# Kernel tuning notes

Measured on AMD Instinct MI355X. Metric: run time of the kernel, lower is better.

Reference implementation:

```python
import jax, jax.numpy as jnp
import numpy as np

B, T, S = 32, 200, 256          # batch, decoder steps, encoder (memory) length
L = 512                          # latent_dims
U = 2 * L                        # LSTM units / attention units / attention_layer_size
E = 512                          # encoder memory feature dim
M = 80                           # mel_bins


def setup_inputs() -> dict:
    key = jax.random.key(0)
    ks = jax.random.split(key, 16)
    s = 0.05
    inputs = jax.random.normal(ks[0], (B, T, M), jnp.float32)
    memory = jax.random.normal(ks[1], (B, S, E), jnp.float32)
    # pre-net: Dense(2L, relu) -> Dropout -> Dense(L, relu) -> Dropout
    W1 = jax.random.normal(ks[2], (M, 2 * L), jnp.float32) * s
    b1 = jnp.zeros((2 * L,), jnp.float32)
    W2 = jax.random.normal(ks[3], (2 * L, L), jnp.float32) * s
    b2 = jnp.zeros((L,), jnp.float32)
    # LSTMCell(2L): input = concat(prenet_out [L], attention [U=2L]) -> 3L
    Wx = jax.random.normal(ks[4], (3 * L, 4 * U), jnp.float32) * s
    Wh = jax.random.normal(ks[5], (U, 4 * U), jnp.float32) * s
    b_lstm = jnp.zeros((4 * U,), jnp.float32)
    # Bahdanau attention (units=U): memory_layer, query_layer (no bias), score vector v
    Wm = jax.random.normal(ks[6], (E, U), jnp.float32) * s
    Wq = jax.random.normal(ks[7], (U, U), jnp.float32) * s
    v_att = jax.random.normal(ks[8], (U,), jnp.float32) * s
    # attention_layer (Dense, no bias): concat(cell_output [U], context [E]) -> U
    Wa = jax.random.normal(ks[9], (U + E, U), jnp.float32) * s
    # output projection to mel bins
    Wp = jax.random.normal(ks[10], (U, M), jnp.float32) * s
    bp = jnp.zeros((M,), jnp.float32)
    return dict(inputs=inputs, memory=memory, W1=W1, b1=b1, W2=W2, b2=b2,
                Wx=Wx, Wh=Wh, b_lstm=b_lstm, Wm=Wm, Wq=Wq, v_att=v_att,
                Wa=Wa, Wp=Wp, bp=bp)


def reference(inputs, memory, W1, b1, W2, b2, Wx, Wh, b_lstm, Wm, Wq, v_att, Wa, Wp, bp):
    # pre-net (inference: dropout is identity)
    x = jax.nn.relu(inputs @ W1 + b1)
    x = jax.nn.relu(x @ W2 + b2)                       # [B,T,L]
    keys = memory @ Wm                                 # precomputed attention keys [B,S,U]

    def step(carry, xt):
        h, c, attn = carry
        cell_in = jnp.concatenate([xt, attn], axis=-1)  # [B, 3L]
        z = cell_in @ Wx + h @ Wh + b_lstm              # [B, 4U]
        i, f, g, o = jnp.split(z, 4, axis=-1)
        c_new = jax.nn.sigmoid(f) * c + jax.nn.sigmoid(i) * jnp.tanh(g)
        h_new = jax.nn.sigmoid(o) * jnp.tanh(c_new)
        # Bahdanau additive attention
        q = h_new @ Wq                                  # [B,U]
        score = jnp.einsum('u,bsu->bs', v_att, jnp.tanh(keys + q[:, None, :]))
        align = jax.nn.softmax(score, axis=-1)          # [B,S]
        ctx = jnp.einsum('bs,bse->be', align, memory)   # [B,E]
        attn_new = jnp.concatenate([h_new, ctx], axis=-1) @ Wa  # [B,U]
        return (h_new, c_new, attn_new), attn_new

    init = (jnp.zeros((B, U), x.dtype), jnp.zeros((B, U), x.dtype), jnp.zeros((B, U), x.dtype))
    xs = jnp.swapaxes(x, 0, 1)                          # [T,B,L]
    (h, c, attn), ys = jax.lax.scan(step, init, xs)
    outs = jnp.swapaxes(ys, 0, 1)                       # [B,T,U]
    mel = outs @ Wp + bp                                # [B,T,M]
    return (mel, h, c, attn)
```

## Files before the change

kernel.cpp:

```cpp
#include <hip/hip_runtime.h>


typedef unsigned short us16;
typedef unsigned int u32;
typedef unsigned long long u64;
typedef __attribute__((ext_vector_type(8))) short bf16x8;
typedef __attribute__((ext_vector_type(4))) float f32x4;

#define MFMA16 __builtin_amdgcn_mfma_f32_16x16x32_bf16
#define AGT __HIP_MEMORY_SCOPE_AGENT

__device__ __forceinline__ us16 f2bf(float f){
  u32 u = __builtin_bit_cast(u32, f);
  u += 0x7fffu + ((u >> 16) & 1u);
  return (us16)(u >> 16);
}
__device__ __forceinline__ float bf2f(us16 h){
  return __builtin_bit_cast(float, ((u32)h) << 16);
}
__device__ __forceinline__ float h2f(us16 u){
  _Float16 h = __builtin_bit_cast(_Float16, u); return (float)h;
}
__device__ __forceinline__ us16 f2h(float f){
  _Float16 h = (_Float16)f; return __builtin_bit_cast(us16, h);
}
__device__ __forceinline__ void split3(float v, us16& s0, us16& s1, us16& s2){
  s0 = f2bf(v); float r = v - bf2f(s0);
  s1 = f2bf(r); r -= bf2f(s1);
  s2 = f2bf(r);
}
__device__ __forceinline__ float tanh_fast(float x){
  float e = __expf(-2.f * fmaxf(x, -40.f));
  return (1.f - e) / (1.f + e);
}
__device__ __forceinline__ float sigf(float x){
  return 1.f / (1.f + __expf(-x));
}

__device__ __forceinline__ u32 aload32(const u32* p){
  return __hip_atomic_load(p, __ATOMIC_RELAXED, AGT);
}
__device__ __forceinline__ void astore16(us16* p, us16 v){
  __hip_atomic_store(p, v, __ATOMIC_RELAXED, AGT);
}
__device__ __forceinline__ void astoref(float* p, float v){
  __hip_atomic_store(p, v, __ATOMIC_RELAXED, AGT);
}
__device__ __forceinline__ void sigflag(u32* p, u32 v){
  __hip_atomic_store(p, v, __ATOMIC_RELAXED, AGT);
}
__device__ __forceinline__ void aaddf(float* p, float v){
  __hip_atomic_fetch_add(p, v, __ATOMIC_RELAXED, AGT);
}
__device__ __forceinline__ bf16x8 ld16(const us16* p){
  return *(const bf16x8*)p;
}
__device__ __forceinline__ bf16x8 pin_reg(bf16x8 v){
  f32x4 t = __builtin_bit_cast(f32x4, v);
  asm volatile("" : "+v"(t));
  return __builtin_bit_cast(bf16x8, t);
}
__device__ __forceinline__ void f32_frag3(const float* p, float rs,
                                          bf16x8& f0, bf16x8& f1, bf16x8& f2){
  float4 t0 = *(const float4*)p;
  float4 t1 = *(const float4*)(p + 4);
  float tf[8] = {t0.x, t0.y, t0.z, t0.w, t1.x, t1.y, t1.z, t1.w};
#pragma unroll
  for (int i = 0; i < 8; ++i){
    float v = tf[i] * rs;
    us16 s0, s1, s2; split3(v, s0, s1, s2);
    f0[i] = (short)s0; f1[i] = (short)s1; f2[i] = (short)s2;
  }
}

#define OFF_WTA    0ull
#define OFF_WQT    50331648ull
#define OFF_X2P    56623104ull
#define OFF_KEYH   76283904ull
#define OFF_KEYL   93061120ull
#define OFF_X1     76283904ull
#define OFF_HIST   109838336ull
#define OFF_HPR    129597440ull
#define OFF_UCR    169115648ull
#define OFF_SR     182288384ull
#define OFF_CB     182314112ull
#define OFF_HF     182445184ull
#define OFF_WAPN   182576256ull
#define OFF_BPERM  182822016ull
#define OFF_ARR    182838400ull
#define OFF_QR     182859776ull
#define TOTAL_WS   209084416ull

#define WTPL 8388608ull
#define WQPL 1048576ull
#define X2PL 3276800ull

__global__ void k_zero_init(u32* hpr0, float* ucr, float* sr, float* cbuf, u32* arr){
  u32 id = blockIdx.x * 256u + threadIdx.x;
  const u32 gs = 65536u;
  for (u32 i = id; i < 49152u;   i += gs) hpr0[i] = 0u;
  for (u32 i = id; i < 3293184u; i += gs) ucr[i]  = 0.f;
  for (u32 i = id; i < 6432u;    i += gs) sr[i]   = (i < 32u) ? 1.f : 0.f;
  for (u32 i = id; i < 32768u;   i += gs) cbuf[i] = 0.f;
  for (u32 i = id; i < 5120u;    i += gs) arr[i]  = 0u;
}

__global__ void k_bperm(const float* __restrict__ bl, float* __restrict__ bpm){
  int c = blockIdx.x * 256 + threadIdx.x;
  if (c < 4096) bpm[((c & 1023) << 2) | (c >> 10)] = bl[c];
}

__global__ void k_transp3(const float* __restrict__ src, us16* __restrict__ dst,
                          int srows, int scols, int ldd, long long pstride, int perm){
  __shared__ float tile[32][33];
  int bx = blockIdx.x * 32, by = blockIdx.y * 32;
  int tx = threadIdx.x & 31, ty = threadIdx.x >> 5;
#pragma unroll
  for (int i = 0; i < 4; ++i){
    int r = by + ty + i * 8, c = bx + tx;
    tile[ty + i * 8][tx] = (r < srows && c < scols) ? src[(size_t)r * scols + c] : 0.f;
  }
  __syncthreads();
#pragma unroll
  for (int i = 0; i < 4; ++i){
    int c = bx + ty + i * 8;
    int r = by + tx;
    if (c < scols && r < srows){
      int oc = perm ? (((c & 1023) << 2) | (c >> 10)) : c;
      float v = tile[tx][ty + i * 8];
      us16 s0, s1, s2; split3(v, s0, s1, s2);
      size_t base = (size_t)oc * ldd + r;
      dst[base] = s0; dst[(size_t)pstride + base] = s1; dst[2ull * pstride + base] = s2;
    }
  }
}

template<int NP, int AF, int BF>
__global__ void __launch_bounds__(256)
k_gemm3(const void* __restrict__ Ap, const void* __restrict__ Bp, void* __restrict__ outp,
        int M, int N, int K, int mode, const float* __restrict__ aux, int ldd){
  __shared__ us16 At[NP][128][72];
  __shared__ us16 Bt[NP][64][72];
  const int tid = threadIdx.x, wv = tid >> 6, lane = tid & 63;
  const int r0 = lane & 15, kg = lane >> 4;
  const int rb = blockIdx.x * 128, cb = blockIdx.y * 64;
  f32x4 acc[2][4];
#pragma unroll
  for (int a = 0; a < 2; ++a)
#pragma unroll
    for (int b = 0; b < 4; ++b) acc[a][b] = (f32x4){0.f, 0.f, 0.f, 0.f};

  const int nkt = (K + 63) >> 6;
  for (int kt = 0; kt < nkt; ++kt){
    const int kb = kt * 64;
    for (int e = tid; e < 8192; e += 256){
      int r = e >> 6, k = e & 63, ga = rb + r, gk = kb + k;
      bool ok = (ga < M) && (gk < K);
      if constexpr (AF){
        float v = ok ? ((const float*)Ap)[(size_t)ga * K + gk] : 0.f;
        us16 s0, s1, s2; split3(v, s0, s1, s2);
        At[0][r][k] = s0;
        if constexpr (NP == 3){ At[1][r][k] = s1; At[2][r][k] = s2; }
      } else {
        At[0][r][k] = ok ? ((const us16*)Ap)[(size_t)ga * K + gk] : (us16)0;
      }
    }
    for (int e = tid; e < 4096; e += 256){
      int kr = e >> 6, c = e & 63, gk = kb + kr, gc = cb + c;
      bool ok = (gk < K) && (gc < N);
      if constexpr (BF){
        float v = ok ? ((const float*)Bp)[(size_t)gk * N + gc] : 0.f;
        us16 s0, s1, s2; split3(v, s0, s1, s2);
        Bt[0][c][kr] = s0;
        if constexpr (NP == 3){ Bt[1][c][kr] = s1; Bt[2][c][kr] = s2; }
      } else {
        Bt[0][c][kr] = ok ? ((const us16*)Bp)[(size_t)gk * N + gc] : (us16)0;
      }
    }
    __syncthreads();
#pragma unroll
    for (int kk = 0; kk < 64; kk += 32){
      bf16x8 af[NP][2];
#pragma unroll
      for (int p = 0; p < NP; ++p){
        af[p][0] = *(const bf16x8*)&At[p][wv * 32 + r0][kk + kg * 8];
        af[p][1] = *(const bf16x8*)&At[p][wv * 32 + 16 + r0][kk + kg * 8];
      }
#pragma unroll
      for (int cf = 0; cf < 4; ++cf){
        bf16x8 bv[NP];
#pragma unroll
        for (int p = 0; p < NP; ++p) bv[p] = *(const bf16x8*)&Bt[p][cf * 16 + r0][kk + kg * 8];
#pragma unroll
        for (int rf = 0; rf < 2; ++rf){
          acc[rf][cf] = MFMA16(af[0][rf], bv[0], acc[rf][cf], 0, 0, 0);
          if constexpr (NP == 3){
            acc[rf][cf] = MFMA16(af[0][rf], bv[1], acc[rf][cf], 0, 0, 0);
            acc[rf][cf] = MFMA16(af[1][rf], bv[0], acc[rf][cf], 0, 0, 0);
            acc[rf][cf] = MFMA16(af[0][rf], bv[2], acc[rf][cf], 0, 0, 0);
            acc[rf][cf] = MFMA16(af[1][rf], bv[1], acc[rf][cf], 0, 0, 0);
            acc[rf][cf] = MFMA16(af[2][rf], bv[0], acc[rf][cf], 0, 0, 0);
          }
        }
      }
    }
    __syncthreads();
  }
  us16* o16 = (us16*)outp; float* of = (float*)outp;
#pragma unroll
  for (int rf = 0; rf < 2; ++rf)
#pragma unroll
    for (int cf = 0; cf < 4; ++cf)
#pragma unroll
      for (int i = 0; i < 4; ++i){
        int r = rb + wv * 32 + rf * 16 + kg * 4 + i;
        int c = cb + cf * 16 + r0;
        if (r >= M || c >= N) continue;
        float v = acc[rf][cf][i];
        if (mode == 0){
          of[(size_t)r * ldd + c] = fmaxf(v + aux[c], 0.f);
        } else if (mode == 1){
          v = fmaxf(v + aux[c], 0.f);
          us16 s0, s1, s2; split3(v, s0, s1, s2);
          size_t b2 = (size_t)r * ldd + c;
          o16[b2] = s0; o16[X2PL + b2] = s1; o16[2 * X2PL + b2] = s2;
        } else if (mode == 2){
          us16 hh = f2h(v); float rem = v - h2f(hh); us16 hl = f2h(rem);
          size_t b2 = (size_t)r * 1024 + c;
          o16[b2] = hh; o16[WTPL + b2] = hl;
        } else if (mode == 3){
          float w = v + (r < 1024 ? aux[(size_t)r * 4096 + c] : 0.f);
          int pc = (c & 1023) * 4 + (c >> 10);
          us16 s0, s1, s2; split3(w, s0, s1, s2);
          size_t b2 = (size_t)pc * 2048 + 512 + r;
          o16[b2] = s0; o16[WTPL + b2] = s1; o16[2 * WTPL + b2] = s2;
        } else if (mode == 4){
          o16[(size_t)r * ldd + c] = f2bf(v);
        } else if (mode == 5){
          of[((size_t)(r & 31) * 200 + (r >> 5)) * 80 + c] = v + aux[c];
        } else {
          of[(size_t)r * ldd + c] = v;
        }
      }
}

__device__ __forceinline__ void gbar3(u32* arr, u32 ep, int tid, int blk){
  asm volatile("s_waitcnt vmcnt(0)" ::: "memory");
  __syncthreads();
  if (blk == 0){
    if (tid > 0 && tid < 256)
      while (aload32(&arr[tid * 16]) < ep) __builtin_amdgcn_s_sleep(2);
    __syncthreads();
    if (tid < 8) sigflag(&arr[4096 + tid * 32], ep);
    __syncthreads();
  } else {
    if (tid == 0){
      sigflag(&arr[blk * 16], ep);
      const int g = blk >> 5;
      while (aload32(&arr[4096 + g * 32]) < ep) __builtin_amdgcn_s_sleep(2);
      __builtin_amdgcn_sched_barrier(0);
    }
    __syncthreads();
  }
}

struct CoopA {
  const us16 *wta, *wqt, *x2p, *kh, *kl;
  const float *mem, *vatt, *bperm;
  us16 *hpr;
  float *ucr, *sr, *qr, *cbuf, *hf32;
  u32 *arr;
};

__global__ void __launch_bounds__(512, 1) k_coop(CoopA a){
  __shared__ us16 khi[32][1024];
  __shared__ us16 klo[32][1024];
  __shared__ float zp[8][512];
  __shared__ float esc[32];
  __shared__ float rs_lds[32];

  __builtin_amdgcn_fence(__ATOMIC_ACQUIRE, "agent");

  const int tid = threadIdx.x, blk = blockIdx.x;
  const int wv = tid >> 6, lane = tid & 63;
  const int r0 = lane & 15, kg = lane >> 4;
  const int cb_b = blk >> 3, cb_s0 = (blk & 7) * 32;
  const int colbase = blk * 16;
  const int u0 = lane * 16;

  bf16x8 wr[8][3];
#pragma unroll
  for (int ks = 0; ks < 8; ++ks){
    const size_t wb = (size_t)(colbase + r0) * 2048 + (size_t)wv * 256 + ks * 32 + kg * 8;
#pragma unroll
    for (int p = 0; p < 3; ++p)
      wr[ks][p] = pin_reg(*(const bf16x8*)&a.wta[(size_t)p * WTPL + wb]);
  }

  {
    const size_t kbase = ((size_t)(cb_b * 256 + cb_s0)) * 1024;
    for (int i = tid; i < 4096; i += 512){
      int r = i >> 7, c8 = (i & 127) * 8;
      *(bf16x8*)&khi[r][c8] = *(const bf16x8*)&a.kh[kbase + (size_t)r * 1024 + c8];
      *(bf16x8*)&klo[r][c8] = *(const bf16x8*)&a.kl[kbase + (size_t)r * 1024 + c8];
    }
  }
  __syncthreads();

  u32 ep = 0;
  for (int t = 0; t < 200; ++t){
    {
      if (tid < 32) rs_lds[tid] = 1.f / a.sr[(size_t)t * 32 + tid];
      __syncthreads();
      f32x4 acc0 = (f32x4){0.f,0.f,0.f,0.f}, acc1 = acc0;
#pragma unroll
      for (int ks = 0; ks < 8; ++ks){
        const int kf = wv * 256 + ks * 32 + kg * 8;
        bf16x8 w0 = wr[ks][0], w1 = wr[ks][1], w2 = wr[ks][2];
        bf16x8 a00, a01, a02, a10, a11, a12;
        if (wv < 2){
          const size_t xb0 = ((size_t)r0 * 200 + t) * 512 + kf;
          const size_t xb1 = ((size_t)(r0 + 16) * 200 + t) * 512 + kf;
          a00 = *(const bf16x8*)&a.x2p[xb0];
          a01 = *(const bf16x8*)&a.x2p[X2PL + xb0];
          a02 = *(const bf16x8*)&a.x2p[2 * X2PL + xb0];
          a10 = *(const bf16x8*)&a.x2p[xb1];
          a11 = *(const bf16x8*)&a.x2p[X2PL + xb1];
          a12 = *(const bf16x8*)&a.x2p[2 * X2PL + xb1];
        } else if (wv < 6){
          const int hk = kf - 512;
          const us16* hb = a.hpr + (size_t)t * 98304;
          a00 = ld16(&hb[(size_t)r0 * 1024 + hk]);
          a01 = ld16(&hb[32768 + (size_t)r0 * 1024 + hk]);
          a02 = ld16(&hb[65536 + (size_t)r0 * 1024 + hk]);
          a10 = ld16(&hb[(size_t)(r0 + 16) * 1024 + hk]);
          a11 = ld16(&hb[32768 + (size_t)(r0 + 16) * 1024 + hk]);
          a12 = ld16(&hb[65536 + (size_t)(r0 + 16) * 1024 + hk]);
        } else {
          const int ek = kf - 1536;
          const float* up = a.ucr + (size_t)t * 16384 + (size_t)r0 * 512 + ek;
          f32_frag3(up,        rs_lds[r0],      a00, a01, a02);
          f32_frag3(up + 8192, rs_lds[r0 + 16], a10, a11, a12);
        }
        acc0 = MFMA16(a00, w0, acc0, 0,0,0); acc0 = MFMA16(a00, w1, acc0, 0,0,0);
        acc0 = MFMA16(a01, w0, acc0, 0,0,0); acc0 = MFMA16(a00, w2, acc0, 0,0,0);
        acc0 = MFMA16(a01, w1, acc0, 0,0,0); acc0 = MFMA16(a02, w0, acc0, 0,0,0);
        acc1 = MFMA16(a10, w0, acc1, 0,0,0); acc1 = MFMA16(a10, w1, acc1, 0,0,0);
        acc1 = MFMA16(a11, w0, acc1, 0,0,0); acc1 = MFMA16(a10, w2, acc1, 0,0,0);
        acc1 = MFMA16(a11, w1, acc1, 0,0,0); acc1 = MFMA16(a12, w0, acc1, 0,0,0);
      }
#pragma unroll
      for (int i = 0; i < 4; ++i){
        zp[wv][(kg * 4 + i) * 16 + r0]      = acc0[i];
        zp[wv][(16 + kg * 4 + i) * 16 + r0] = acc1[i];
      }
      __syncthreads();
      float z = 0.f;
#pragma unroll
      for (int w = 0; w < 8; ++w) z += zp[w][tid];
      z += a.bperm[colbase + (tid & 15)];
      __syncthreads();
      zp[0][tid] = z;
      __syncthreads();
      if (tid < 128){
        int b = tid >> 2, ul = tid & 3, u = blk * 4 + ul;
        float zi = zp[0][b * 16 + ul * 4 + 0];
        float zf = zp[0][b * 16 + ul * 4 + 1];
        float zg = zp[0][b * 16 + ul * 4 + 2];
        float zo = zp[0][b * 16 + ul * 4 + 3];
        float co = a.cbuf[b * 1024 + u];
        float cn = sigf(zf) * co + sigf(zi) * tanh_fast(zg);
        float hn = sigf(zo) * tanh_fast(cn);
        a.cbuf[b * 1024 + u] = cn;
        a.hf32[b * 1024 + u] = hn;
        us16 s0, s1, s2; split3(hn, s0, s1, s2);
        us16* hb = a.hpr + (size_t)(t + 1) * 98304;
        astore16(&hb[b * 1024 + u], s0);
        astore16(&hb[32768 + b * 1024 + u], s1);
        astore16(&hb[65536 + b * 1024 + u], s2);
      }
    }
    gbar3(a.arr, ++ep, tid, blk);

    if (blk < 64){
      f32x4 acc0 = (f32x4){0.f,0.f,0.f,0.f}, acc1 = acc0;
#pragma unroll
      for (int ks = 0; ks < 4; ++ks){
        const int kf = wv * 128 + ks * 32 + kg * 8;
        const size_t wb = (size_t)(colbase + r0) * 1024 + kf;
        bf16x8 w0 = *(const bf16x8*)&a.wqt[wb];
        bf16x8 w1 = *(const bf16x8*)&a.wqt[WQPL + wb];
        bf16x8 w2 = *(const bf16x8*)&a.wqt[2 * WQPL + wb];
        const us16* hb = a.hpr + (size_t)(t + 1) * 98304;
        bf16x8 a00 = ld16(&hb[(size_t)r0 * 1024 + kf]);
        bf16x8 a01 = ld16(&hb[32768 + (size_t)r0 * 1024 + kf]);
        bf16x8 a02 = ld16(&hb[65536 + (size_t)r0 * 1024 + kf]);
        bf16x8 a10 = ld16(&hb[(size_t)(r0 + 16) * 1024 + kf]);
        bf16x8 a11 = ld16(&hb[32768 + (size_t)(r0 + 16) * 1024 + kf]);
        bf16x8 a12 = ld16(&hb[65536 + (size_t)(r0 + 16) * 1024 + kf]);
        acc0 = MFMA16(a00, w0, acc0, 0,0,0); acc0 = MFMA16(a00, w1, acc0, 0,0,0);
        acc0 = MFMA16(a01, w0, acc0, 0,0,0); acc0 = MFMA16(a00, w2, acc0, 0,0,0);
        acc0 = MFMA16(a01, w1, acc0, 0,0,0); acc0 = MFMA16(a02, w0, acc0, 0,0,0);
        acc1 = MFMA16(a10, w0, acc1, 0,0,0); acc1 = MFMA16(a10, w1, acc1, 0,0,0);
        acc1 = MFMA16(a11, w0, acc1, 0,0,0); acc1 = MFMA16(a10, w2, acc1, 0,0,0);
        acc1 = MFMA16(a11, w1, acc1, 0,0,0); acc1 = MFMA16(a12, w0, acc1, 0,0,0);
      }
#pragma unroll
      for (int i = 0; i < 4; ++i){
        zp[wv][(kg * 4 + i) * 16 + r0]      = acc0[i];
        zp[wv][(16 + kg * 4 + i) * 16 + r0] = acc1[i];
      }
      __syncthreads();
      float q = 0.f;
#pragma unroll
      for (int w = 0; w < 8; ++w) q += zp[w][tid];
      astoref(&a.qr[(size_t)t * 32768 + (size_t)(tid >> 4) * 1024 + colbase + (tid & 15)], q);
    }
    gbar3(a.arr, ++ep, tid, blk);

    {
      float qv[16], vv[16];
      {
        const float* qp = a.qr + (size_t)t * 32768 + (size_t)cb_b * 1024 + u0;
        float4 q0 = *(const float4*)qp;
        float4 q1 = *(const float4*)(qp + 4);
        float4 q2 = *(const float4*)(qp + 8);
        float4 q3 = *(const float4*)(qp + 12);
        qv[0]=q0.x; qv[1]=q0.y; qv[2]=q0.z; qv[3]=q0.w;
        qv[4]=q1.x; qv[5]=q1.y; qv[6]=q1.z; qv[7]=q1.w;
        qv[8]=q2.x; qv[9]=q2.y; qv[10]=q2.z; qv[11]=q2.w;
        qv[12]=q3.x; qv[13]=q3.y; qv[14]=q3.z; qv[15]=q3.w;
        float4 v0 = *(const float4*)(a.vatt + u0);
        float4 v1 = *(const float4*)(a.vatt + u0 + 4);
        float4 v2 = *(const float4*)(a.vatt + u0 + 8);
        float4 v3 = *(const float4*)(a.vatt + u0 + 12);
        vv[0]=v0.x; vv[1]=v0.y; vv[2]=v0.z; vv[3]=v0.w;
        vv[4]=v1.x; vv[5]=v1.y; vv[6]=v1.z; vv[7]=v1.w;
        vv[8]=v2.x; vv[9]=v2.y; vv[10]=v2.z; vv[11]=v2.w;
        vv[12]=v3.x; vv[13]=v3.y; vv[14]=v3.z; vv[15]=v3.w;
      }
#pragma unroll
      for (int m = 0; m < 4; ++m){
        const int sl = wv * 4 + m;
        bf16x8 h0 = *(const bf16x8*)&khi[sl][u0];
        bf16x8 h1 = *(const bf16x8*)&khi[sl][u0 + 8];
        bf16x8 l0 = *(const bf16x8*)&klo[sl][u0];
        bf16x8 l1 = *(const bf16x8*)&klo[sl][u0 + 8];
        float part = 0.f;
#pragma unroll
        for (int j = 0; j < 8; ++j){
          float kva = h2f((us16)h0[j]) + h2f((us16)l0[j]);
          part += vv[j] * tanh_fast(kva + qv[j]);
          float kvb = h2f((us16)h1[j]) + h2f((us16)l1[j]);
          part += vv[8 + j] * tanh_fast(kvb + qv[8 + j]);
        }
#pragma unroll
        for (int off = 32; off; off >>= 1) part += __shfl_xor(part, off);
        if (lane == 0) esc[sl] = __expf(part);
      }
      __syncthreads();
      if (tid == 0){
        float bs = 0.f;
#pragma unroll
        for (int i = 0; i < 32; ++i) bs += esc[i];
        aaddf(&a.sr[(size_t)(t + 1) * 32 + cb_b], bs);
      }
      {
        float ac0 = 0.f, ac1 = 0.f, ac2 = 0.f, ac3 = 0.f;
        const float* mrow = a.mem + ((size_t)(cb_b * 256 + cb_s0)) * 512 + tid;
#pragma unroll
        for (int j = 0; j < 32; j += 4){
          ac0 += esc[j]     * mrow[(size_t)j * 512];
          ac1 += esc[j + 1] * mrow[(size_t)(j + 1) * 512];
          ac2 += esc[j + 2] * mrow[(size_t)(j + 2) * 512];
          ac3 += esc[j + 3] * mrow[(size_t)(j + 3) * 512];
        }
        aaddf(&a.ucr[(size_t)(t + 1) * 16384 + cb_b * 512 + tid], (ac0 + ac1) + (ac2 + ac3));
      }
    }
    gbar3(a.arr, ++ep, tid, blk);
  }
}

__global__ void k_hist(const us16* __restrict__ hpr, const float* __restrict__ ucr,
                       const float* __restrict__ sr, us16* __restrict__ hist){
  int row = blockIdx.x;
  int t = row >> 5, b = row & 31;
  float rs = 1.f / sr[(size_t)t * 32 + b];
  for (int c = threadIdx.x; c < 1536; c += 256){
    us16 v;
    if (c < 1024) v = hpr[(size_t)t * 98304 + b * 1024 + c];
    else          v = f2bf(ucr[(size_t)t * 16384 + b * 512 + (c - 1024)] * rs);
    hist[(size_t)row * 1536 + c] = v;
  }
}

__global__ void k_copy_hc(const float* __restrict__ h, const float* __restrict__ c,
                          float* __restrict__ out){
  int i = blockIdx.x * 256 + threadIdx.x;
  if (i < 32768){
    out[512000 + i] = h[i];
    out[544768 + i] = c[i];
  }
}

extern "C" void kernel_launch(void* const* d_in, const int* in_sizes, int n_in,
                              void* d_out, int out_size, void* d_ws, size_t ws_size,
                              hipStream_t stream){
  const float* inputs = (const float*)d_in[0];
  const float* memory = (const float*)d_in[1];
  const float* W1     = (const float*)d_in[2];
  const float* b1     = (const float*)d_in[3];
  const float* W2     = (const float*)d_in[4];
  const float* b2     = (const float*)d_in[5];
  const float* Wx     = (const float*)d_in[6];
  const float* Wh     = (const float*)d_in[7];
  const float* b_lstm = (const float*)d_in[8];
  const float* Wm     = (const float*)d_in[9];
  const float* Wq     = (const float*)d_in[10];
  const float* v_att  = (const float*)d_in[11];
  const float* Wa     = (const float*)d_in[12];
  const float* Wp     = (const float*)d_in[13];
  const float* bp     = (const float*)d_in[14];
  float* out = (float*)d_out;
  char* ws = (char*)d_ws;
  if (ws_size < TOTAL_WS) return;

  us16* WTA    = (us16*)(ws + OFF_WTA);
  us16* WQT    = (us16*)(ws + OFF_WQT);
  us16* X2P    = (us16*)(ws + OFF_X2P);
  us16* KEYH   = (us16*)(ws + OFF_KEYH);
  float* X1    = (float*)(ws + OFF_X1);
  us16* HIST   = (us16*)(ws + OFF_HIST);
  us16* HPR    = (us16*)(ws + OFF_HPR);
  float* UCR   = (float*)(ws + OFF_UCR);
  float* SR    = (float*)(ws + OFF_SR);
  float* QR    = (float*)(ws + OFF_QR);
  float* CB    = (float*)(ws + OFF_CB);
  float* HF    = (float*)(ws + OFF_HF);
  us16* WAPN   = (us16*)(ws + OFF_WAPN);
  float* BPM   = (float*)(ws + OFF_BPERM);
  u32*  ARR    = (u32*)(ws + OFF_ARR);

  k_zero_init<<<256, 256, 0, stream>>>((u32*)HPR, UCR, SR, CB, ARR);
  k_bperm<<<16, 256, 0, stream>>>(b_lstm, BPM);
  k_transp3<<<dim3(32, 32), 256, 0, stream>>>(Wq, WQT, 1024, 1024, 1024, (long long)WQPL, 0);
  k_transp3<<<dim3(128, 16), 256, 0, stream>>>(Wx, WTA, 512, 4096, 2048, (long long)WTPL, 1);

  k_gemm3<3,1,1><<<dim3(12, 64), 256, 0, stream>>>(Wa, Wx + (size_t)512 * 4096, WTA,
                                                   1536, 4096, 1024, 3, Wh, 0);
  k_gemm3<3,1,1><<<dim3(12, 2), 256, 0, stream>>>(Wa, Wp, WAPN, 1536, 80, 1024, 4, nullptr, 80);
  k_gemm3<3,1,1><<<dim3(50, 16), 256, 0, stream>>>(inputs, W1, X1, 6400, 1024, 80, 0, b1, 1024);
  k_gemm3<3,1,1><<<dim3(50, 8), 256, 0, stream>>>(X1, W2, X2P, 6400, 512, 1024, 1, b2, 512);
  k_gemm3<3,1,1><<<dim3(64, 16), 256, 0, stream>>>(memory, Wm, KEYH, 8192, 1024, 512, 2, nullptr, 1024);

  CoopA ca;
  ca.wta = WTA; ca.wqt = WQT; ca.x2p = X2P; ca.kh = KEYH; ca.kl = KEYH + WTPL;
  ca.mem = memory; ca.vatt = v_att; ca.bperm = BPM;
  ca.hpr = HPR; ca.ucr = UCR; ca.sr = SR;
  ca.qr = QR; ca.cbuf = CB; ca.hf32 = HF; ca.arr = ARR;
  void* args[] = {(void*)&ca};
  hipLaunchCooperativeKernel((const void*)k_coop, dim3(256), dim3(512), args, 0, stream);

  k_hist<<<6432, 256, 0, stream>>>(HPR, UCR, SR, HIST);
  k_gemm3<1,0,0><<<dim3(50, 2), 256, 0, stream>>>(HIST + (size_t)32 * 1536, WAPN, out,
                                                  6400, 80, 1536, 5, bp, 0);
  k_gemm3<1,0,1><<<dim3(1, 16), 256, 0, stream>>>(HIST + (size_t)200 * 32 * 1536, Wa,
                                                  out + 577536, 32, 1024, 1536, 6, nullptr, 1024);
  k_copy_hc<<<128, 256, 0, stream>>>(HF, CB, out);
}
```

Measured before the change: 12.58 ms.

## Split batch into two halves and pipeline phases with per-phase split barriers

Replaces the global three-phase barrier per timestep with arrive/wait counters per phase and per batch half. Each phase (LSTM gates, query projection, attention) runs on two 16-row halves, so one half's work can overlap with the other half's barrier latency. The Wq projection is now spread over 128 blocks instead of 64, and the attention block mapping is re-tiled to 16 positions by 2 batch groups. The cost is more barriers, MFMA tiles half as tall, which may underuse the matrix units, and extra LDS syncs.

```diff
diff --git a/kernel.cpp b/kernel.cpp
--- a/kernel.cpp
+++ b/kernel.cpp
@@ -88,12 +88,19 @@
 #define OFF_WAPN   182576256ull
 #define OFF_BPERM  182822016ull
 #define OFF_ARR    182838400ull
-#define OFF_QR     182859776ull
-#define TOTAL_WS   209084416ull
+#define OFF_QR     182870016ull
+#define TOTAL_WS   209094656ull
 
 #define WTPL 8388608ull
 #define WQPL 1048576ull
 #define X2PL 3276800ull
+
+#define SA0 0
+#define SA1 1
+#define SB0 2
+#define SB1 3
+#define SC0 4
+#define SC1 5
 
 __global__ void k_zero_init(u32* hpr0, float* ucr, float* sr, float* cbuf, u32* arr){
   u32 id = blockIdx.x * 256u + threadIdx.x;
@@ -102,7 +109,7 @@
   for (u32 i = id; i < 3293184u; i += gs) ucr[i]  = 0.f;
   for (u32 i = id; i < 6432u;    i += gs) sr[i]   = (i < 32u) ? 1.f : 0.f;
   for (u32 i = id; i < 32768u;   i += gs) cbuf[i] = 0.f;
-  for (u32 i = id; i < 5120u;    i += gs) arr[i]  = 0u;
+  for (u32 i = id; i < 2048u;    i += gs) arr[i]  = 0u;
 }
 
 __global__ void k_bperm(const float* __restrict__ bl, float* __restrict__ bpm){
@@ -244,24 +251,24 @@
       }
 }
 
-__device__ __forceinline__ void gbar3(u32* arr, u32 ep, int tid, int blk){
-  asm volatile("s_waitcnt vmcnt(0)" ::: "memory");
+__device__ __forceinline__ void arrv(u32* arr, int set, u32 ng, u32 ep, int tid, int blk){
   __syncthreads();
-  if (blk == 0){
-    if (tid > 0 && tid < 256)
-      while (aload32(&arr[tid * 16]) < ep) __builtin_amdgcn_s_sleep(2);
-    __syncthreads();
-    if (tid < 8) sigflag(&arr[4096 + tid * 32], ep);
-    __syncthreads();
-  } else {
-    if (tid == 0){
-      sigflag(&arr[blk * 16], ep);
-      const int g = blk >> 5;
-      while (aload32(&arr[4096 + g * 32]) < ep) __builtin_amdgcn_s_sleep(2);
-      __builtin_amdgcn_sched_barrier(0);
-    }
-    __syncthreads();
-  }
+  if (tid == 0){
+    int g = (blk >> 5) & 7;
+    u32 old = __hip_atomic_fetch_add(&arr[(set * 8 + g) * 32], 1u, __ATOMIC_RELAXED, AGT);
+    if (old == 32u * ep - 1u){
+      u32 r = __hip_atomic_fetch_add(&arr[(48 + set) * 32], 1u, __ATOMIC_RELAXED, AGT);
+      if (r == ng * ep - 1u)
+        sigflag(&arr[(56 + set) * 32], ep);
+    }
+  }
+}
+__device__ __forceinline__ void waitrel(u32* arr, int set, u32 ep, int tid){
+  if (tid == 0){
+    while (aload32(&arr[(56 + set) * 32]) < ep) __builtin_amdgcn_s_sleep(2);
+    __builtin_amdgcn_sched_barrier(0);
+  }
+  __syncthreads();
 }
 
 struct CoopA {
@@ -276,7 +283,7 @@
   __shared__ us16 khi[32][1024];
   __shared__ us16 klo[32][1024];
   __shared__ float zp[8][512];
-  __shared__ float esc[32];
+  __shared__ float esc[16];
   __shared__ float rs_lds[32];
 
   __builtin_amdgcn_fence(__ATOMIC_ACQUIRE, "agent");
@@ -284,7 +291,7 @@
   const int tid = threadIdx.x, blk = blockIdx.x;
   const int wv = tid >> 6, lane = tid & 63;
   const int r0 = lane & 15, kg = lane >> 4;
-  const int cb_b = blk >> 3, cb_s0 = (blk & 7) * 32;
+  const int b16 = blk >> 4, s0c = (blk & 15) * 16;
   const int colbase = blk * 16;
   const int u0 = lane * 16;
 
@@ -298,187 +305,191 @@
   }
 
   {
-    const size_t kbase = ((size_t)(cb_b * 256 + cb_s0)) * 1024;
     for (int i = tid; i < 4096; i += 512){
       int r = i >> 7, c8 = (i & 127) * 8;
-      *(bf16x8*)&khi[r][c8] = *(const bf16x8*)&a.kh[kbase + (size_t)r * 1024 + c8];
-      *(bf16x8*)&klo[r][c8] = *(const bf16x8*)&a.kl[kbase + (size_t)r * 1024 + c8];
+      int gb = (r < 16) ? b16 : (16 + b16);
+      int s  = s0c + (r & 15);
+      const size_t kb = ((size_t)(gb * 256 + s)) * 1024 + c8;
+      *(bf16x8*)&khi[r][c8] = *(const bf16x8*)&a.kh[kb];
+      *(bf16x8*)&klo[r][c8] = *(const bf16x8*)&a.kl[kb];
     }
   }
   __syncthreads();
 
-  u32 ep = 0;
-  for (int t = 0; t < 200; ++t){
-    {
-      if (tid < 32) rs_lds[tid] = 1.f / a.sr[(size_t)t * 32 + tid];
-      __syncthreads();
-      f32x4 acc0 = (f32x4){0.f,0.f,0.f,0.f}, acc1 = acc0;
-#pragma unroll
-      for (int ks = 0; ks < 8; ++ks){
-        const int kf = wv * 256 + ks * 32 + kg * 8;
-        bf16x8 w0 = wr[ks][0], w1 = wr[ks][1], w2 = wr[ks][2];
-        bf16x8 a00, a01, a02, a10, a11, a12;
-        if (wv < 2){
-          const size_t xb0 = ((size_t)r0 * 200 + t) * 512 + kf;
-          const size_t xb1 = ((size_t)(r0 + 16) * 200 + t) * 512 + kf;
-          a00 = *(const bf16x8*)&a.x2p[xb0];
-          a01 = *(const bf16x8*)&a.x2p[X2PL + xb0];
-          a02 = *(const bf16x8*)&a.x2p[2 * X2PL + xb0];
-          a10 = *(const bf16x8*)&a.x2p[xb1];
-          a11 = *(const bf16x8*)&a.x2p[X2PL + xb1];
-          a12 = *(const bf16x8*)&a.x2p[2 * X2PL + xb1];
-        } else if (wv < 6){
-          const int hk = kf - 512;
-          const us16* hb = a.hpr + (size_t)t * 98304;
-          a00 = ld16(&hb[(size_t)r0 * 1024 + hk]);
-          a01 = ld16(&hb[32768 + (size_t)r0 * 1024 + hk]);
-          a02 = ld16(&hb[65536 + (size_t)r0 * 1024 + hk]);
-          a10 = ld16(&hb[(size_t)(r0 + 16) * 1024 + hk]);
-          a11 = ld16(&hb[32768 + (size_t)(r0 + 16) * 1024 + hk]);
-          a12 = ld16(&hb[65536 + (size_t)(r0 + 16) * 1024 + hk]);
-        } else {
-          const int ek = kf - 1536;
-          const float* up = a.ucr + (size_t)t * 16384 + (size_t)r0 * 512 + ek;
-          f32_frag3(up,        rs_lds[r0],      a00, a01, a02);
-          f32_frag3(up + 8192, rs_lds[r0 + 16], a10, a11, a12);
-        }
-        acc0 = MFMA16(a00, w0, acc0, 0,0,0); acc0 = MFMA16(a00, w1, acc0, 0,0,0);
-        acc0 = MFMA16(a01, w0, acc0, 0,0,0); acc0 = MFMA16(a00, w2, acc0, 0,0,0);
-        acc0 = MFMA16(a01, w1, acc0, 0,0,0); acc0 = MFMA16(a02, w0, acc0, 0,0,0);
-        acc1 = MFMA16(a10, w0, acc1, 0,0,0); acc1 = MFMA16(a10, w1, acc1, 0,0,0);
-        acc1 = MFMA16(a11, w0, acc1, 0,0,0); acc1 = MFMA16(a10, w2, acc1, 0,0,0);
-        acc1 = MFMA16(a11, w1, acc1, 0,0,0); acc1 = MFMA16(a12, w0, acc1, 0,0,0);
-      }
-#pragma unroll
-      for (int i = 0; i < 4; ++i){
-        zp[wv][(kg * 4 + i) * 16 + r0]      = acc0[i];
-        zp[wv][(16 + kg * 4 + i) * 16 + r0] = acc1[i];
-      }
-      __syncthreads();
-      float z = 0.f;
+  auto phaseA = [&](int g, int t){
+    if (tid < 16) rs_lds[g * 16 + tid] = 1.f / a.sr[(size_t)t * 32 + g * 16 + tid];
+    __syncthreads();
+    const int gr = g * 16;
+    f32x4 acc = (f32x4){0.f, 0.f, 0.f, 0.f};
+#pragma unroll
+    for (int ks = 0; ks < 8; ++ks){
+      const int kf = wv * 256 + ks * 32 + kg * 8;
+      bf16x8 w0 = wr[ks][0], w1 = wr[ks][1], w2 = wr[ks][2];
+      bf16x8 a0, a1, a2;
+      if (wv < 2){
+        const size_t xb = ((size_t)(gr + r0) * 200 + t) * 512 + kf;
+        a0 = *(const bf16x8*)&a.x2p[xb];
+        a1 = *(const bf16x8*)&a.x2p[X2PL + xb];
+        a2 = *(const bf16x8*)&a.x2p[2 * X2PL + xb];
+      } else if (wv < 6){
+        const int hk = kf - 512;
+        const us16* hb = a.hpr + (size_t)t * 98304 + (size_t)(gr + r0) * 1024 + hk;
+        a0 = ld16(hb); a1 = ld16(hb + 32768); a2 = ld16(hb + 65536);
+      } else {
+        const int ek = kf - 1536;
+        const float* up = a.ucr + (size_t)t * 16384 + (size_t)(gr + r0) * 512 + ek;
+        f32_frag3(up, rs_lds[gr + r0], a0, a1, a2);
+      }
+      acc = MFMA16(a0, w0, acc, 0,0,0); acc = MFMA16(a0, w1, acc, 0,0,0);
+      acc = MFMA16(a1, w0, acc, 0,0,0); acc = MFMA16(a0, w2, acc, 0,0,0);
+      acc = MFMA16(a1, w1, acc, 0,0,0); acc = MFMA16(a2, w0, acc, 0,0,0);
+    }
+#pragma unroll
+    for (int i = 0; i < 4; ++i)
+      zp[wv][(kg * 4 + i) * 16 + r0] = acc[i];
+    __syncthreads();
+    float z = 0.f;
+    if (tid < 256){
 #pragma unroll
       for (int w = 0; w < 8; ++w) z += zp[w][tid];
       z += a.bperm[colbase + (tid & 15)];
-      __syncthreads();
-      zp[0][tid] = z;
-      __syncthreads();
-      if (tid < 128){
-        int b = tid >> 2, ul = tid & 3, u = blk * 4 + ul;
-        float zi = zp[0][b * 16 + ul * 4 + 0];
-        float zf = zp[0][b * 16 + ul * 4 + 1];
-        float zg = zp[0][b * 16 + ul * 4 + 2];
-        float zo = zp[0][b * 16 + ul * 4 + 3];
-        float co = a.cbuf[b * 1024 + u];
-        float cn = sigf(zf) * co + sigf(zi) * tanh_fast(zg);
-        float hn = sigf(zo) * tanh_fast(cn);
-        a.cbuf[b * 1024 + u] = cn;
-        a.hf32[b * 1024 + u] = hn;
-        us16 s0, s1, s2; split3(hn, s0, s1, s2);
-        us16* hb = a.hpr + (size_t)(t + 1) * 98304;
-        astore16(&hb[b * 1024 + u], s0);
-        astore16(&hb[32768 + b * 1024 + u], s1);
-        astore16(&hb[65536 + b * 1024 + u], s2);
-      }
-    }
-    gbar3(a.arr, ++ep, tid, blk);
-
+    }
+    __syncthreads();
+    if (tid < 256) zp[0][tid] = z;
+    __syncthreads();
+    if (tid < 64){
+      int bl = tid >> 2, ul = tid & 3, u = blk * 4 + ul;
+      int b = gr + bl;
+      float zi = zp[0][bl * 16 + ul * 4 + 0];
+      float zf = zp[0][bl * 16 + ul * 4 + 1];
+      float zg = zp[0][bl * 16 + ul * 4 + 2];
+      float zo = zp[0][bl * 16 + ul * 4 + 3];
+      float co = a.cbuf[b * 1024 + u];
+      float cn = sigf(zf) * co + sigf(zi) * tanh_fast(zg);
+      float hn = sigf(zo) * tanh_fast(cn);
+      a.cbuf[b * 1024 + u] = cn;
+      a.hf32[b * 1024 + u] = hn;
+      us16 s0, s1, s2; split3(hn, s0, s1, s2);
+      us16* hb = a.hpr + (size_t)(t + 1) * 98304 + b * 1024 + u;
+      astore16(hb, s0);
+      astore16(hb + 32768, s1);
+      astore16(hb + 65536, s2);
+    }
+  };
+
+  auto phaseB = [&](int g, int t, int colb){
+    const int gr = g * 16;
+    f32x4 acc = (f32x4){0.f, 0.f, 0.f, 0.f};
+#pragma unroll
+    for (int ks = 0; ks < 4; ++ks){
+      const int kf = wv * 128 + ks * 32 + kg * 8;
+      const size_t wb = (size_t)(colb + r0) * 1024 + kf;
+      bf16x8 w0 = *(const bf16x8*)&a.wqt[wb];
+      bf16x8 w1 = *(const bf16x8*)&a.wqt[WQPL + wb];
+      bf16x8 w2 = *(const bf16x8*)&a.wqt[2 * WQPL + wb];
+      const us16* hb = a.hpr + (size_t)(t + 1) * 98304 + (size_t)(gr + r0) * 1024 + kf;
+      bf16x8 a0 = ld16(hb), a1 = ld16(hb + 32768), a2 = ld16(hb + 65536);
+      acc = MFMA16(a0, w0, acc, 0,0,0); acc = MFMA16(a0, w1, acc, 0,0,0);
+      acc = MFMA16(a1, w0, acc, 0,0,0); acc = MFMA16(a0, w2, acc, 0,0,0);
+      acc = MFMA16(a1, w1, acc, 0,0,0); acc = MFMA16(a2, w0, acc, 0,0,0);
+    }
+#pragma unroll
+    for (int i = 0; i < 4; ++i)
+      zp[wv][(kg * 4 + i) * 16 + r0] = acc[i];
+    __syncthreads();
+    if (tid < 256){
+      float q = 0.f;
+#pragma unroll
+      for (int w = 0; w < 8; ++w) q += zp[w][tid];
+      astoref(&a.qr[(size_t)t * 32768 + (size_t)(gr + (tid >> 4)) * 1024 + colb + (tid & 15)], q);
+    }
+  };
+
+  auto phaseC = [&](int g, int t){
+    const int b = g * 16 + b16;
+    float qv[16], vv[16];
+    {
+      const float* qp = a.qr + (size_t)t * 32768 + (size_t)b * 1024 + u0;
+      float4 q0 = *(const float4*)qp;
+      float4 q1 = *(const float4*)(qp + 4);
+      float4 q2 = *(const float4*)(qp + 8);
+      float4 q3 = *(const float4*)(qp + 12);
+      qv[0]=q0.x; qv[1]=q0.y; qv[2]=q0.z; qv[3]=q0.w;
+      qv[4]=q1.x; qv[5]=q1.y; qv[6]=q1.z; qv[7]=q1.w;
+      qv[8]=q2.x; qv[9]=q2.y; qv[10]=q2.z; qv[11]=q2.w;
+      qv[12]=q3.x; qv[13]=q3.y; qv[14]=q3.z; qv[15]=q3.w;
+      float4 v0 = *(const float4*)(a.vatt + u0);
+      float4 v1 = *(const float4*)(a.vatt + u0 + 4);
+      float4 v2 = *(const float4*)(a.vatt + u0 + 8);
+      float4 v3 = *(const float4*)(a.vatt + u0 + 12);
+      vv[0]=v0.x; vv[1]=v0.y; vv[2]=v0.z; vv[3]=v0.w;
+      vv[4]=v1.x; vv[5]=v1.y; vv[6]=v1.z; vv[7]=v1.w;
+      vv[8]=v2.x; vv[9]=v2.y; vv[10]=v2.z; vv[11]=v2.w;
+      vv[12]=v3.x; vv[13]=v3.y; vv[14]=v3.z; vv[15]=v3.w;
+    }
+#pragma unroll
+    for (int m = 0; m < 2; ++m){
+      const int sl = wv * 2 + m;
+      const int kr = g * 16 + sl;
+      bf16x8 h0 = *(const bf16x8*)&khi[kr][u0];
+      bf16x8 h1 = *(const bf16x8*)&khi[kr][u0 + 8];
+      bf16x8 l0 = *(const bf16x8*)&klo[kr][u0];
+      bf16x8 l1 = *(const bf16x8*)&klo[kr][u0 + 8];
+      float part = 0.f;
+#pragma unroll
+      for (int j = 0; j < 8; ++j){
+        float kva = h2f((us16)h0[j]) + h2f((us16)l0[j]);
+        part += vv[j] * tanh_fast(kva + qv[j]);
+        float kvb = h2f((us16)h1[j]) + h2f((us16)l1[j]);
+        part += vv[8 + j] * tanh_fast(kvb + qv[8 + j]);
+      }
+#pragma unroll
+      for (int off = 32; off; off >>= 1) part += __shfl_xor(part, off);
+      if (lane == 0) esc[sl] = __expf(part);
+    }
+    __syncthreads();
+    if (tid == 0){
+      float bs = 0.f;
+#pragma unroll
+      for (int i = 0; i < 16; ++i) bs += esc[i];
+      aaddf(&a.sr[(size_t)(t + 1) * 32 + b], bs);
+    }
+    {
+      float ac0 = 0.f, ac1 = 0.f;
+      const float* mrow = a.mem + ((size_t)(b * 256 + s0c)) * 512 + tid;
+#pragma unroll
+      for (int j = 0; j < 16; j += 2){
+        ac0 += esc[j]     * mrow[(size_t)j * 512];
+        ac1 += esc[j + 1] * mrow[(size_t)(j + 1) * 512];
+      }
+      aaddf(&a.ucr[(size_t)(t + 1) * 16384 + b * 512 + tid], ac0 + ac1);
+    }
+    __syncthreads();
+  };
+
+  for (int t = 0; t < 200; ++t){
+    const u32 ep = (u32)(t + 1);
+    waitrel(a.arr, SC0, (u32)t, tid);
+    phaseA(0, t);
+    arrv(a.arr, SA0, 8, ep, tid, blk);
+    waitrel(a.arr, SC1, (u32)t, tid);
+    phaseA(1, t);
+    arrv(a.arr, SA1, 8, ep, tid, blk);
     if (blk < 64){
-      f32x4 acc0 = (f32x4){0.f,0.f,0.f,0.f}, acc1 = acc0;
-#pragma unroll
-      for (int ks = 0; ks < 4; ++ks){
-        const int kf = wv * 128 + ks * 32 + kg * 8;
-        const size_t wb = (size_t)(colbase + r0) * 1024 + kf;
-        bf16x8 w0 = *(const bf16x8*)&a.wqt[wb];
-        bf16x8 w1 = *(const bf16x8*)&a.wqt[WQPL + wb];
-        bf16x8 w2 = *(const bf16x8*)&a.wqt[2 * WQPL + wb];
-        const us16* hb = a.hpr + (size_t)(t + 1) * 98304;
-        bf16x8 a00 = ld16(&hb[(size_t)r0 * 1024 + kf]);
-        bf16x8 a01 = ld16(&hb[32768 + (size_t)r0 * 1024 + kf]);
-        bf16x8 a02 = ld16(&hb[65536 + (size_t)r0 * 1024 + kf]);
-        bf16x8 a10 = ld16(&hb[(size_t)(r0 + 16) * 1024 + kf]);
-        bf16x8 a11 = ld16(&hb[32768 + (size_t)(r0 + 16) * 1024 + kf]);
-        bf16x8 a12 = ld16(&hb[65536 + (size_t)(r0 + 16) * 1024 + kf]);
-        acc0 = MFMA16(a00, w0, acc0, 0,0,0); acc0 = MFMA16(a00, w1, acc0, 0,0,0);
-        acc0 = MFMA16(a01, w0, acc0, 0,0,0); acc0 = MFMA16(a00, w2, acc0, 0,0,0);
-        acc0 = MFMA16(a01, w1, acc0, 0,0,0); acc0 = MFMA16(a02, w0, acc0, 0,0,0);
-        acc1 = MFMA16(a10, w0, acc1, 0,0,0); acc1 = MFMA16(a10, w1, acc1, 0,0,0);
-        acc1 = MFMA16(a11, w0, acc1, 0,0,0); acc1 = MFMA16(a10, w2, acc1, 0,0,0);
-        acc1 = MFMA16(a11, w1, acc1, 0,0,0); acc1 = MFMA16(a12, w0, acc1, 0,0,0);
-      }
-#pragma unroll
-      for (int i = 0; i < 4; ++i){
-        zp[wv][(kg * 4 + i) * 16 + r0]      = acc0[i];
-        zp[wv][(16 + kg * 4 + i) * 16 + r0] = acc1[i];
-      }
-      __syncthreads();
-      float q = 0.f;
-#pragma unroll
-      for (int w = 0; w < 8; ++w) q += zp[w][tid];
-      astoref(&a.qr[(size_t)t * 32768 + (size_t)(tid >> 4) * 1024 + colbase + (tid & 15)], q);
-    }
-    gbar3(a.arr, ++ep, tid, blk);
-
-    {
-      float qv[16], vv[16];
-      {
-        const float* qp = a.qr + (size_t)t * 32768 + (size_t)cb_b * 1024 + u0;
-        float4 q0 = *(const float4*)qp;
-        float4 q1 = *(const float4*)(qp + 4);
-        float4 q2 = *(const float4*)(qp + 8);
-        float4 q3 = *(const float4*)(qp + 12);
-        qv[0]=q0.x; qv[1]=q0.y; qv[2]=q0.z; qv[3]=q0.w;
-        qv[4]=q1.x; qv[5]=q1.y; qv[6]=q1.z; qv[7]=q1.w;
-        qv[8]=q2.x; qv[9]=q2.y; qv[10]=q2.z; qv[11]=q2.w;
-        qv[12]=q3.x; qv[13]=q3.y; qv[14]=q3.z; qv[15]=q3.w;
-        float4 v0 = *(const float4*)(a.vatt + u0);
-        float4 v1 = *(const float4*)(a.vatt + u0 + 4);
-        float4 v2 = *(const float4*)(a.vatt + u0 + 8);
-        float4 v3 = *(const float4*)(a.vatt + u0 + 12);
-        vv[0]=v0.x; vv[1]=v0.y; vv[2]=v0.z; vv[3]=v0.w;
-        vv[4]=v1.x; vv[5]=v1.y; vv[6]=v1.z; vv[7]=v1.w;
-        vv[8]=v2.x; vv[9]=v2.y; vv[10]=v2.z; vv[11]=v2.w;
-        vv[12]=v3.x; vv[13]=v3.y; vv[14]=v3.z; vv[15]=v3.w;
-      }
-#pragma unroll
-      for (int m = 0; m < 4; ++m){
-        const int sl = wv * 4 + m;
-        bf16x8 h0 = *(const bf16x8*)&khi[sl][u0];
-        bf16x8 h1 = *(const bf16x8*)&khi[sl][u0 + 8];
-        bf16x8 l0 = *(const bf16x8*)&klo[sl][u0];
-        bf16x8 l1 = *(const bf16x8*)&klo[sl][u0 + 8];
-        float part = 0.f;
-#pragma unroll
-        for (int j = 0; j < 8; ++j){
-          float kva = h2f((us16)h0[j]) + h2f((us16)l0[j]);
-          part += vv[j] * tanh_fast(kva + qv[j]);
-          float kvb = h2f((us16)h1[j]) + h2f((us16)l1[j]);
-          part += vv[8 + j] * tanh_fast(kvb + qv[8 + j]);
-        }
-#pragma unroll
-        for (int off = 32; off; off >>= 1) part += __shfl_xor(part, off);
-        if (lane == 0) esc[sl] = __expf(part);
-      }
-      __syncthreads();
-      if (tid == 0){
-        float bs = 0.f;
-#pragma unroll
-        for (int i = 0; i < 32; ++i) bs += esc[i];
-        aaddf(&a.sr[(size_t)(t + 1) * 32 + cb_b], bs);
-      }
-      {
-        float ac0 = 0.f, ac1 = 0.f, ac2 = 0.f, ac3 = 0.f;
-        const float* mrow = a.mem + ((size_t)(cb_b * 256 + cb_s0)) * 512 + tid;
-#pragma unroll
-        for (int j = 0; j < 32; j += 4){
-          ac0 += esc[j]     * mrow[(size_t)j * 512];
-          ac1 += esc[j + 1] * mrow[(size_t)(j + 1) * 512];
-          ac2 += esc[j + 2] * mrow[(size_t)(j + 2) * 512];
-          ac3 += esc[j + 3] * mrow[(size_t)(j + 3) * 512];
-        }
-        aaddf(&a.ucr[(size_t)(t + 1) * 16384 + cb_b * 512 + tid], (ac0 + ac1) + (ac2 + ac3));
-      }
-    }
-    gbar3(a.arr, ++ep, tid, blk);
+      waitrel(a.arr, SA0, ep, tid);
+      phaseB(0, t, blk * 16);
+      arrv(a.arr, SB0, 2, ep, tid, blk);
+    } else if (blk < 128){
+      waitrel(a.arr, SA1, ep, tid);
+      phaseB(1, t, (blk - 64) * 16);
+      arrv(a.arr, SB1, 2, ep, tid, blk);
+    }
+    waitrel(a.arr, SB0, ep, tid);
+    phaseC(0, t);
+    arrv(a.arr, SC0, 8, ep, tid, blk);
+    waitrel(a.arr, SB1, ep, tid);
+    phaseC(1, t);
+    arrv(a.arr, SC1, 8, ep, tid, blk);
   }
 }
 
```

After: 11.85 ms. -5.8%, faster.
